# Optimization experiments

Hardware: AMD Instinct MI355X
Metric: run time of the kernel (lower is better)

The kernel has to match this reference:

```python
import jax, jax.numpy as jnp
import numpy as np


def _run_stacked_lstm(x, init_hc, params):
    """x: [B,T,E]; init_hc: tuple of (h,c) per layer; params: tuple of (W,U,b) per layer.
    Keras LSTMCell gate order: i, f, g(candidate), o; sigmoid recurrent act, tanh act."""
    def step(carry, xt):
        inp = xt
        new = []
        for (h, c), (W, U, b) in zip(carry, params):
            z = inp @ W + h @ U + b                      # [B, 4*units]
            i, f, g, o = jnp.split(z, 4, axis=-1)
            c2 = jax.nn.sigmoid(f) * c + jax.nn.sigmoid(i) * jnp.tanh(g)
            h2 = jax.nn.sigmoid(o) * jnp.tanh(c2)
            new.append((h2, c2))
            inp = h2                                     # feed to next layer
        return tuple(new), inp
    carry, ys = jax.lax.scan(step, init_hc, jnp.swapaxes(x, 0, 1))
    return jnp.swapaxes(ys, 0, 1), carry                 # [B,T,units], final states


def setup_inputs() -> dict:
    key = jax.random.key(0)
    ks = jax.random.split(key, 20)
    B, T, V, E, H, L = 16, 64, 32000, 512, 512, 2
    s = 0.02
    inp = {
        'ids_1': jax.random.randint(ks[0], (B, T), 0, V),
        'ids_2': jax.random.randint(ks[1], (B, T), 0, V),
        'init_state': jax.random.normal(ks[2], (L, B, H), jnp.float32),
        'emb': jax.random.normal(ks[3], (V, E), jnp.float32) * s,
        'W1_0': jax.random.normal(ks[4], (E, 4 * H), jnp.float32) * s,
        'U1_0': jax.random.normal(ks[5], (H, 4 * H), jnp.float32) * s,
        'b1_0': jnp.zeros((4 * H,), jnp.float32),
        'W1_1': jax.random.normal(ks[6], (H, 4 * H), jnp.float32) * s,
        'U1_1': jax.random.normal(ks[7], (H, 4 * H), jnp.float32) * s,
        'b1_1': jnp.zeros((4 * H,), jnp.float32),
        'W2_0': jax.random.normal(ks[8], (E, 8 * H), jnp.float32) * s,
        'U2_0': jax.random.normal(ks[9], (2 * H, 8 * H), jnp.float32) * s,
        'b2_0': jnp.zeros((8 * H,), jnp.float32),
        'W2_1': jax.random.normal(ks[10], (2 * H, 8 * H), jnp.float32) * s,
        'U2_1': jax.random.normal(ks[11], (2 * H, 8 * H), jnp.float32) * s,
        'b2_1': jnp.zeros((8 * H,), jnp.float32),
        'Wp1': jax.random.normal(ks[12], (H, V), jnp.float32) * s,
        'bp1': jnp.zeros((V,), jnp.float32),
        'Wp2': jax.random.normal(ks[13], (2 * H, V), jnp.float32) * s,
        'bp2': jnp.zeros((V,), jnp.float32),
    }
    return inp


def reference(ids_1, ids_2, init_state, emb,
              W1_0, U1_0, b1_0, W1_1, U1_1, b1_1,
              W2_0, U2_0, b2_0, W2_1, U2_1, b2_1,
              Wp1, bp1, Wp2, bp2):
    L = init_state.shape[0]
    e1 = emb[ids_1]                                       # [B,T,E]
    e2 = emb[ids_2]
    # RNN1: initial (h,c) both set to init_state per layer
    init1 = tuple((init_state[l], init_state[l]) for l in range(L))
    p1 = ((W1_0, U1_0, b1_0), (W1_1, U1_1, b1_1))
    out1, st1 = _run_stacked_lstm(e1, init1, p1)
    logits1 = out1 @ Wp1 + bp1                            # [B,T,V]
    # RNN2: initial h = concat(init, h1_final), c = concat(init, c1_final)
    init2 = tuple((jnp.concatenate([init_state[l], st1[l][0]], axis=1),
                   jnp.concatenate([init_state[l], st1[l][1]], axis=1))
                  for l in range(L))
    p2 = ((W2_0, U2_0, b2_0), (W2_1, U2_1, b2_1))
    out2, _ = _run_stacked_lstm(e2, init2, p2)
    logits2 = out2 @ Wp2 + bp2                            # [B,T,V]
    return (logits1, logits2)
```

## Files before the change

### kernel.cpp

```cpp
#include <hip/hip_runtime.h>
#include <hip/hip_bf16.h>

#define B_ 16
#define T_ 64
#define E_ 512
#define H_ 512
#define V_ 32000

typedef __attribute__((ext_vector_type(4))) float f32x4;
typedef __attribute__((ext_vector_type(8))) short s16x8;

__device__ __forceinline__ float sigm(float x){ return 1.0f/(1.0f + __expf(-x)); }

__device__ __forceinline__ unsigned short f2bf(float x){
  unsigned int u = __float_as_uint(x);
  return (unsigned short)((u + 0x7FFFu + ((u>>16)&1u)) >> 16);
}

__device__ __forceinline__ unsigned load_coh(const unsigned* p){
  unsigned v;
  asm volatile("global_load_dword %0, %1, off sc0 sc1\n\ts_waitcnt vmcnt(0)"
               : "=v"(v) : "v"(p) : "memory");
  return v;
}
__device__ __forceinline__ void store_coh16(unsigned short* p, unsigned v){
  asm volatile("global_store_short %0, %1, off sc0 sc1" :: "v"(p), "v"(v) : "memory");
}
__device__ __forceinline__ void store_cohf(float* p, float v){
  asm volatile("global_store_dword %0, %1, off sc0 sc1" :: "v"(p), "v"(v) : "memory");
}

__device__ __forceinline__ void gbar2(unsigned* barb, unsigned bi1,
                                      unsigned grp, unsigned grpcnt){
  asm volatile("s_waitcnt vmcnt(0)" ::: "memory");
  __syncthreads();
  if(threadIdx.x == 0){
    unsigned* ctr = barb + (size_t)grp*64;
    unsigned* mst = barb + (size_t)8*64;
    unsigned* gen = barb + (size_t)9*64;
    unsigned a = __hip_atomic_fetch_add(ctr, 1u, __ATOMIC_RELAXED, __HIP_MEMORY_SCOPE_AGENT);
    if(a == bi1*grpcnt - 1u){
      unsigned m = __hip_atomic_fetch_add(mst, 1u, __ATOMIC_RELAXED, __HIP_MEMORY_SCOPE_AGENT);
      if(m == bi1*8u - 1u){
        asm volatile("global_store_dword %0, %1, off sc0 sc1\n\ts_waitcnt vmcnt(0)"
                     :: "v"(gen), "v"(bi1) : "memory");
      }
    }
    while(load_coh(gen) < bi1) __builtin_amdgcn_s_sleep(1);
  }
  __syncthreads();
}

__global__ void k_barinit(unsigned* bar){
  int i = blockIdx.x*256 + threadIdx.x;
  if(i < 2048) bar[i] = 0u;
}

__global__ void k_gather(const int* __restrict__ ids, const float* __restrict__ emb,
                         unsigned short* __restrict__ out){
  const int row = blockIdx.x;
  const int id  = ids[row];
  float4 v = *(const float4*)(emb + (size_t)id*E_ + threadIdx.x*4);
  ushort4 o;
  o.x = f2bf(v.x); o.y = f2bf(v.y); o.z = f2bf(v.z); o.w = f2bf(v.w);
  *(ushort4*)(out + (size_t)row*E_ + threadIdx.x*4) = o;
}

__global__ __launch_bounds__(256)
void k_tcvt(const float* __restrict__ in, unsigned short* __restrict__ out,
            int N, int Hp, int Kfull, int koff, int swz){
  __shared__ float tile[32][33];
  const int n0 = blockIdx.x*32, k0 = blockIdx.y*32;
  const int x = threadIdx.x & 31, y = threadIdx.x >> 5;
  #pragma unroll
  for(int i=0;i<4;i++){
    int k = y + i*8;
    tile[k][x] = in[(size_t)(k0+k)*N + n0 + x];
  }
  __syncthreads();
  #pragma unroll
  for(int i=0;i<4;i++){
    int nl = y + i*8;
    int n  = n0 + nl;
    int p  = Hp ? ((n % Hp)*4 + n / Hp) : n;
    int kk = koff + k0 + x;
    size_t idx;
    if(swz){
      int k2 = kk*2;
      int slot = ((k2>>4)&7) ^ (p&7);
      idx = (size_t)p*Kfull + (((k2 & ~127) | (slot<<4) | (k2 & 15)) >> 1);
    } else {
      idx = (size_t)p*Kfull + kk;
    }
    out[idx] = f2bf(tile[x][nl]);
  }
}

__global__ void k_bpack(const float* __restrict__ b, float* __restrict__ out, int H, int N){
  int p = blockIdx.x*256 + threadIdx.x;
  if(p < N) out[p] = b[(p&3)*H + (p>>2)];
}

__global__ void k_init1(const float* __restrict__ init_state,
                        unsigned short* h0i, float* c0i, unsigned short* h1i, float* c1i){
  int i = blockIdx.x*256 + threadIdx.x;
  if(i >= B_*H_) return;
  float v0 = init_state[i];
  float v1 = init_state[B_*H_ + i];
  h0i[i] = f2bf(v0); c0i[i] = v0;
  h1i[i] = f2bf(v1); c1i[i] = v1;
}

__global__ void k_init2(const float* __restrict__ init_state,
                        const unsigned short* __restrict__ h0seq1,
                        const unsigned short* __restrict__ h1seq1,
                        const float* __restrict__ c0f1, const float* __restrict__ c1f1,
                        unsigned short* h20i, unsigned short* h21i,
                        float* c20i, float* c21i){
  const int l = blockIdx.y;
  int i = blockIdx.x*256 + threadIdx.x;
  if(i >= B_*2*H_) return;
  const int r = i >> 10, j = i & 1023;
  unsigned short* ho = l ? h21i : h20i;
  float* co = l ? c21i : c20i;
  if(j < H_){
    float v = init_state[(size_t)l*B_*H_ + r*H_ + j];
    ho[i] = f2bf(v); co[i] = v;
  } else {
    const unsigned short* hs = l ? h1seq1 : h0seq1;
    const float* cf = l ? c1f1 : c0f1;
    ho[i] = hs[(size_t)(r*T_ + (T_-1))*H_ + (j - H_)];
    co[i] = cf[r*H_ + (j - H_)];
  }
}

template<int BF32>
__global__ __launch_bounds__(256)
void k_mm(const unsigned short* __restrict__ A, const void* __restrict__ Bsrc,
          const float* __restrict__ bias, float* __restrict__ C,
          int M, int N, int K){
  __shared__ __align__(16) unsigned short As[128*64];
  __shared__ __align__(16) unsigned short Bs[128*64];
  const int tid = threadIdx.x;
  const int lane = tid & 63, w = tid >> 6;
  const int wm = (w>>1)*64, wn = (w&1)*64;
  const int bm = blockIdx.y*128, bn = blockIdx.x*128;
  const int l15 = lane & 15, kg = lane >> 4;
  f32x4 acc[4][4] = {};

  for(int k0=0; k0<K; k0+=64){
    __syncthreads();
    #pragma unroll
    for(int ch=0; ch<4; ch++){
      int off = ch*4096 + tid*16;
      int row = off >> 7;
      int s   = ((off >> 4) & 7) ^ (row & 7);
      __builtin_amdgcn_global_load_lds(
        (const __attribute__((address_space(1))) unsigned int*)(A + (size_t)(bm+row)*K + k0 + s*8),
        (__attribute__((address_space(3))) unsigned int*)((char*)As + off), 16, 0, 0);
    }
    if(BF32){
      const float* Bf = (const float*)Bsrc;
      #pragma unroll
      for(int i=0;i<8;i++){
        int kl = (tid>>5) + i*8;
        int nl = (tid&31)*4;
        float4 v = *(const float4*)(Bf + (size_t)(k0+kl)*N + bn + nl);
        int slot = kl >> 3, kb = kl & 7;
        float vv[4] = {v.x, v.y, v.z, v.w};
        #pragma unroll
        for(int jj=0;jj<4;jj++){
          int n = nl + jj;
          Bs[n*64 + ((slot ^ (n&7))*8) + kb] = f2bf(vv[jj]);
        }
      }
    } else {
      const unsigned short* Bt = (const unsigned short*)Bsrc;
      #pragma unroll
      for(int ch=0; ch<4; ch++){
        int off = ch*4096 + tid*16;
        int row = off >> 7;
        int s   = ((off >> 4) & 7) ^ (row & 7);
        __builtin_amdgcn_global_load_lds(
          (const __attribute__((address_space(1))) unsigned int*)(Bt + (size_t)(bn+row)*K + k0 + s*8),
          (__attribute__((address_space(3))) unsigned int*)((char*)Bs + off), 16, 0, 0);
      }
    }
    __syncthreads();

    #pragma unroll
    for(int q=0;q<2;q++){
      s16x8 af[4], bf[4];
      #pragma unroll
      for(int mt=0;mt<4;mt++){
        int row = wm + mt*16 + l15;
        int s = (q*4 + kg) ^ (row & 7);
        af[mt] = *(const s16x8*)(As + row*64 + s*8);
      }
      #pragma unroll
      for(int nt=0;nt<4;nt++){
        int row = wn + nt*16 + l15;
        int s = (q*4 + kg) ^ (row & 7);
        bf[nt] = *(const s16x8*)(Bs + row*64 + s*8);
      }
      #pragma unroll
      for(int mt=0;mt<4;mt++)
        #pragma unroll
        for(int nt=0;nt<4;nt++)
          acc[mt][nt] = __builtin_amdgcn_mfma_f32_16x16x32_bf16(af[mt], bf[nt], acc[mt][nt], 0, 0, 0);
    }
  }
  #pragma unroll
  for(int mt=0;mt<4;mt++){
    #pragma unroll
    for(int nt=0;nt<4;nt++){
      int col = bn + wn + nt*16 + l15;
      float bv = bias ? bias[col] : 0.f;
      #pragma unroll
      for(int e=0;e<4;e++){
        int row = bm + wm + mt*16 + kg*4 + e;
        C[(size_t)row*N + col] = acc[mt][nt][e] + bv;
      }
    }
  }
}

template<int C, int K, int LAYER, int HU>
__device__ __forceinline__ void rnn_body(
    unsigned short* __restrict__ Uld, float* __restrict__ zp,
    const unsigned short* __restrict__ Uslice,
    const float* __restrict__ xw0, const float* __restrict__ bpk,
    const unsigned short* __restrict__ h0init, const unsigned short* __restrict__ h1init,
    const float* __restrict__ cinit,
    unsigned short* __restrict__ h0seq, unsigned short* __restrict__ h1seq,
    float* __restrict__ cfin, unsigned* bar, int cb,
    unsigned grp, unsigned grpcnt)
{
  constexpr int KW = K/4, KS = KW/32, FR = C/16, UB = C/4;
  constexpr int K2 = K*2;
  constexpr int ITEMS = 16*UB;
  const int tid = threadIdx.x;
  const int lane = tid & 63, w = tid >> 6;
  const int l15 = lane & 15, kg = lane >> 4;

  constexpr int CP = (C*K2)/4096;
  #pragma unroll
  for(int i=0;i<CP;i++){
    __builtin_amdgcn_global_load_lds(
      (const __attribute__((address_space(1))) unsigned int*)((const char*)Uslice + i*4096 + tid*16),
      (__attribute__((address_space(3))) unsigned int*)((char*)Uld + i*4096 + tid*16), 16, 0, 0);
  }
  const int base_p = cb*C;
  const int base_u = cb*UB;
  float4 bvr = make_float4(0.f,0.f,0.f,0.f);
  int er = 0, eu = 0;
  if(tid < ITEMS){ er = tid / UB; eu = tid - er*UB; bvr = *(const float4*)(bpk + base_p + eu*4); }
  float creg = 0.f;
  unsigned short* hseqW = LAYER ? h1seq : h0seq;

  int cbyte[FR], cx[FR];
  #pragma unroll
  for(int f=0;f<FR;f++){ int c = f*16 + l15; cbyte[f] = c*K2; cx[f] = (c&7)<<4; }

  __syncthreads();

  for(int it = 0; it <= T_; ++it){
    const bool active = LAYER ? (it >= 1) : (it < T_);
    const int t = LAYER ? it-1 : it;
    if(active){
      const unsigned short* asrc;
      if constexpr(LAYER == 0){
        asrc = (t == 0) ? (h0init + l15*HU)
                        : (h0seq + ((size_t)(l15*T_ + (t-1)))*HU);
      } else {
        if(w < 2){
          asrc = h0seq + ((size_t)(l15*T_ + t))*HU;
        } else {
          asrc = ((t == 0) ? (h1init + l15*HU)
                           : (h1seq + ((size_t)(l15*T_ + (t-1)))*HU)) - HU;
        }
      }
      f32x4 acc[FR];
      #pragma unroll
      for(int f=0;f<FR;f++) acc[f] = (f32x4){0.f,0.f,0.f,0.f};
      #pragma unroll
      for(int s=0;s<KS;s++){
        const int kel = w*KW + s*32 + kg*8;
        s16x8 a = *(const s16x8*)(asrc + kel);
        const int kb  = kel*2;
        const int kch = kb & ~127;
        const int ksl = (kb >> 4) & 7;
        #pragma unroll
        for(int f=0;f<FR;f++){
          const int ad = cbyte[f] + kch + ((ksl<<4) ^ cx[f]);
          s16x8 b = *(const s16x8*)((const char*)Uld + ad);
          acc[f] = __builtin_amdgcn_mfma_f32_16x16x32_bf16(a, b, acc[f], 0, 0, 0);
        }
      }
      #pragma unroll
      for(int f=0;f<FR;f++)
        #pragma unroll
        for(int e=0;e<4;e++)
          zp[(w*16 + kg*4 + e)*68 + f*16 + l15] = acc[f][e];
    }
    __syncthreads();
    if(active && tid < ITEMS){
      float4 z0 = *(const float4*)(zp + (     er)*68 + eu*4);
      float4 z1 = *(const float4*)(zp + (16 + er)*68 + eu*4);
      float4 z2 = *(const float4*)(zp + (32 + er)*68 + eu*4);
      float4 z3 = *(const float4*)(zp + (48 + er)*68 + eu*4);
      float si = z0.x+z1.x+z2.x+z3.x + bvr.x;
      float sf = z0.y+z1.y+z2.y+z3.y + bvr.y;
      float sg = z0.z+z1.z+z2.z+z3.z + bvr.z;
      float so = z0.w+z1.w+z2.w+z3.w + bvr.w;
      if constexpr(LAYER == 0){
        float4 xv = *(const float4*)(xw0 + ((size_t)(er*T_ + t))*(4*HU) + base_p + eu*4);
        si += xv.x; sf += xv.y; sg += xv.z; so += xv.w;
      }
      float cin = (t == 0) ? cinit[er*HU + base_u + eu] : creg;
      float c2 = sigm(sf)*cin + sigm(si)*tanhf(sg);
      float h2 = sigm(so)*tanhf(c2);
      creg = c2;
      store_coh16(&hseqW[((size_t)(er*T_ + t))*HU + base_u + eu], (unsigned)f2bf(h2));
      if(t == T_-1) store_cohf(&cfin[er*HU + base_u + eu], c2);
    }
    if(it < T_) gbar2(bar, (unsigned)(it+1), grp, grpcnt);
  }
}

template<int HU, int C0, int C1>
__global__ __launch_bounds__(256, 1)
void k_rnn(const unsigned short* __restrict__ Ut0, const unsigned short* __restrict__ WU1,
           const float* __restrict__ xw0, const float* __restrict__ bpk0, const float* __restrict__ bpk1,
           const unsigned short* __restrict__ h0init, const unsigned short* __restrict__ h1init,
           const float* __restrict__ c0init, const float* __restrict__ c1init,
           unsigned short* __restrict__ h0seq, unsigned short* __restrict__ h1seq,
           float* __restrict__ c0fin, float* __restrict__ c1fin, unsigned* bar)
{
  constexpr int NB0 = 4*HU/C0;
  constexpr int UMAXE = (C0*HU > C1*2*HU) ? C0*HU : C1*2*HU;
  __shared__ __align__(16) unsigned short Uld[UMAXE];
  __shared__ __align__(16) float zred[64*68];
  const unsigned grp = blockIdx.x & 7u;
  const unsigned grpcnt = gridDim.x >> 3;
  const int blk = blockIdx.x;
  if(blk < NB0)
    rnn_body<C0, HU, 0, HU>(Uld, zred, Ut0 + (size_t)blk*C0*HU, xw0, bpk0,
                            h0init, h1init, c0init, h0seq, h1seq, c0fin, bar, blk, grp, grpcnt);
  else
    rnn_body<C1, 2*HU, 1, HU>(Uld, zred, WU1 + (size_t)(blk-NB0)*C1*2*HU, nullptr, bpk1,
                            h0init, h1init, c1init, h0seq, h1seq, c1fin, bar, blk-NB0, grp, grpcnt);
}

extern "C" void kernel_launch(void* const* d_in, const int* in_sizes, int n_in,
                              void* d_out, int out_size, void* d_ws, size_t ws_size,
                              hipStream_t stream){
  const int*   ids1 = (const int*)d_in[0];
  const int*   ids2 = (const int*)d_in[1];
  const float* init = (const float*)d_in[2];
  const float* emb  = (const float*)d_in[3];
  const float* W1_0 = (const float*)d_in[4];
  const float* U1_0 = (const float*)d_in[5];
  const float* b1_0 = (const float*)d_in[6];
  const float* W1_1 = (const float*)d_in[7];
  const float* U1_1 = (const float*)d_in[8];
  const float* b1_1 = (const float*)d_in[9];
  const float* W2_0 = (const float*)d_in[10];
  const float* U2_0 = (const float*)d_in[11];
  const float* b2_0 = (const float*)d_in[12];
  const float* W2_1 = (const float*)d_in[13];
  const float* U2_1 = (const float*)d_in[14];
  const float* b2_1 = (const float*)d_in[15];
  const float* Wp1  = (const float*)d_in[16];
  const float* bp1  = (const float*)d_in[17];
  const float* Wp2  = (const float*)d_in[18];
  const float* bp2  = (const float*)d_in[19];
  float* out1 = (float*)d_out;
  float* out2 = out1 + (size_t)B_*T_*V_;

  char* base = (char*)d_ws;
  float*          xw    = (float*)(base);
  unsigned short* ut0_1 = (unsigned short*)(base + (16u<<20));
  unsigned short* wu1_1 = (unsigned short*)(base + (18u<<20));
  unsigned short* ut0_2 = (unsigned short*)(base + (22u<<20));
  unsigned short* wu1_2 = (unsigned short*)(base + (30u<<20));
  unsigned short* wtmp  = (unsigned short*)(base + (46u<<20));
  unsigned short* ebuf  = (unsigned short*)(base + (50u<<20));
  unsigned short* h0s1  = (unsigned short*)(base + (51u<<20));
  unsigned short* h1s1  = (unsigned short*)(base + (52u<<20));
  unsigned short* h0s2  = (unsigned short*)(base + (53u<<20));
  unsigned short* h1s2  = (unsigned short*)(base + (55u<<20));
  char* M = base + (57u<<20);
  unsigned short* h0i1 = (unsigned short*)(M);
  unsigned short* h1i1 = (unsigned short*)(M + 16384);
  float* c0i1 = (float*)(M + 32768);
  float* c1i1 = (float*)(M + 65536);
  unsigned short* h2i0 = (unsigned short*)(M + 98304);
  unsigned short* h2i1 = (unsigned short*)(M + 131072);
  float* c2i0 = (float*)(M + 163840);
  float* c2i1 = (float*)(M + 229376);
  float* c0f1 = (float*)(M + 294912);
  float* c1f1 = (float*)(M + 327680);
  float* c0f2 = (float*)(M + 360448);
  float* c1f2 = (float*)(M + 425984);
  float* bpk10 = (float*)(M + 491520);
  float* bpk11 = (float*)(M + 499712);
  float* bpk20 = (float*)(M + 507904);
  float* bpk21 = (float*)(M + 524288);
  unsigned* bar1 = (unsigned*)(M + 540672);
  unsigned* bar2 = (unsigned*)(M + 544768);
  unsigned short* wpT = (unsigned short*)(base + (58u<<20));
  const size_t NEED_ALL = ((size_t)58u<<20) + (size_t)V_*1024*2;
  const bool wide = ws_size >= NEED_ALL;

  k_barinit<<<dim3(8), dim3(256), 0, stream>>>(bar1);

  k_init1<<<dim3(32), dim3(256), 0, stream>>>(init, h0i1, c0i1, h1i1, c1i1);
  k_gather<<<dim3(B_*T_), dim3(128), 0, stream>>>(ids1, emb, ebuf);
  k_tcvt<<<dim3(64, 16), dim3(256), 0, stream>>>(U1_0, ut0_1, 2048, 512, 512, 0, 1);
  k_tcvt<<<dim3(64, 16), dim3(256), 0, stream>>>(W1_0, wtmp,  2048, 512, 512, 0, 0);
  k_tcvt<<<dim3(64, 16), dim3(256), 0, stream>>>(W1_1, wu1_1, 2048, 512, 1024, 0, 1);
  k_tcvt<<<dim3(64, 16), dim3(256), 0, stream>>>(U1_1, wu1_1, 2048, 512, 1024, 512, 1);
  k_bpack<<<dim3(8),  dim3(256), 0, stream>>>(b1_0, bpk10, 512, 2048);
  k_bpack<<<dim3(8),  dim3(256), 0, stream>>>(b1_1, bpk11, 512, 2048);
  k_mm<0><<<dim3(16, 8), dim3(256), 0, stream>>>(ebuf, wtmp, nullptr, xw, 1024, 2048, 512);
  k_rnn<512, 64, 64><<<dim3(64), dim3(256), 0, stream>>>(ut0_1, wu1_1, xw, bpk10, bpk11,
      h0i1, h1i1, c0i1, c1i1, h0s1, h1s1, c0f1, c1f1, bar1);
  if(wide){
    k_tcvt<<<dim3(1000, 16), dim3(256), 0, stream>>>(Wp1, wpT, V_, 0, 512, 0, 0);
    k_mm<0><<<dim3(250, 8), dim3(256), 0, stream>>>(h1s1, wpT, bp1, out1, 1024, V_, 512);
  } else {
    k_mm<1><<<dim3(250, 8), dim3(256), 0, stream>>>(h1s1, Wp1, bp1, out1, 1024, V_, 512);
  }

  k_init2<<<dim3(64, 2), dim3(256), 0, stream>>>(init, h0s1, h1s1, c0f1, c1f1,
                                                 h2i0, h2i1, c2i0, c2i1);
  k_gather<<<dim3(B_*T_), dim3(128), 0, stream>>>(ids2, emb, ebuf);
  k_tcvt<<<dim3(128, 32), dim3(256), 0, stream>>>(U2_0, ut0_2, 4096, 1024, 1024, 0, 1);
  k_tcvt<<<dim3(128, 16), dim3(256), 0, stream>>>(W2_0, wtmp,  4096, 1024, 512, 0, 0);
  k_tcvt<<<dim3(128, 32), dim3(256), 0, stream>>>(W2_1, wu1_2, 4096, 1024, 2048, 0, 1);
  k_tcvt<<<dim3(128, 32), dim3(256), 0, stream>>>(U2_1, wu1_2, 4096, 1024, 2048, 1024, 1);
  k_bpack<<<dim3(16), dim3(256), 0, stream>>>(b2_0, bpk20, 1024, 4096);
  k_bpack<<<dim3(16), dim3(256), 0, stream>>>(b2_1, bpk21, 1024, 4096);
  k_mm<0><<<dim3(32, 8), dim3(256), 0, stream>>>(ebuf, wtmp, nullptr, xw, 1024, 4096, 512);
  k_rnn<1024, 64, 32><<<dim3(192), dim3(256), 0, stream>>>(ut0_2, wu1_2, xw, bpk20, bpk21,
      h2i0, h2i1, c2i0, c2i1, h0s2, h1s2, c0f2, c1f2, bar2);
  if(wide){
    k_tcvt<<<dim3(1000, 32), dim3(256), 0, stream>>>(Wp2, wpT, V_, 0, 1024, 0, 0);
    k_mm<0><<<dim3(250, 8), dim3(256), 0, stream>>>(h1s2, wpT, bp2, out2, 1024, V_, 1024);
  } else {
    k_mm<1><<<dim3(250, 8), dim3(256), 0, stream>>>(h1s2, Wp2, bp2, out2, 1024, V_, 1024);
  }
}
```

Measured before the change: 934.3 us.

## Replace grid-wide barrier with per-block progress flags and column-split recurrent GEMV

The global two-level atomic barrier between timesteps is replaced by per-block monotonic progress flags that consumers poll for just the producers they depend on. Layer 0 and layer 1 now advance as a dataflow pipeline instead of lockstep, with layer 1 waiting on layer 0's flag for the same step. Layer 0 and the small RNN's layer 1 also switch to a column-split scheme where each wave owns whole columns and gates are combined with lane shuffles, which removes the LDS split-K reduction and one __syncthreads per step. In exchange, every wave polls many flags with coherent loads, adding memory traffic and added complexity around ordering.

```diff
diff --git a/kernel.cpp b/kernel.cpp
--- a/kernel.cpp
+++ b/kernel.cpp
@@ -29,26 +29,22 @@
 __device__ __forceinline__ void store_cohf(float* p, float v){
   asm volatile("global_store_dword %0, %1, off sc0 sc1" :: "v"(p), "v"(v) : "memory");
 }
-
-__device__ __forceinline__ void gbar2(unsigned* barb, unsigned bi1,
-                                      unsigned grp, unsigned grpcnt){
-  asm volatile("s_waitcnt vmcnt(0)" ::: "memory");
-  __syncthreads();
-  if(threadIdx.x == 0){
-    unsigned* ctr = barb + (size_t)grp*64;
-    unsigned* mst = barb + (size_t)8*64;
-    unsigned* gen = barb + (size_t)9*64;
-    unsigned a = __hip_atomic_fetch_add(ctr, 1u, __ATOMIC_RELAXED, __HIP_MEMORY_SCOPE_AGENT);
-    if(a == bi1*grpcnt - 1u){
-      unsigned m = __hip_atomic_fetch_add(mst, 1u, __ATOMIC_RELAXED, __HIP_MEMORY_SCOPE_AGENT);
-      if(m == bi1*8u - 1u){
-        asm volatile("global_store_dword %0, %1, off sc0 sc1\n\ts_waitcnt vmcnt(0)"
-                     :: "v"(gen), "v"(bi1) : "memory");
-      }
-    }
-    while(load_coh(gen) < bi1) __builtin_amdgcn_s_sleep(1);
-  }
-  __syncthreads();
+__device__ __forceinline__ void store_cohu(unsigned* p, unsigned v){
+  asm volatile("global_store_dword %0, %1, off sc0 sc1" :: "v"(p), "v"(v) : "memory");
+}
+
+template<int NF>
+__device__ __forceinline__ void pollge(const unsigned* flags, unsigned target){
+  const int lane = threadIdx.x & 63;
+  if constexpr(NF <= 64){
+    const unsigned* p = flags + (lane % NF);
+    while(load_coh(p) < target) __builtin_amdgcn_s_sleep(1);
+  } else {
+    const unsigned* p0 = flags + lane;
+    const unsigned* p1 = flags + 64 + lane;
+    while(load_coh(p0) < target) __builtin_amdgcn_s_sleep(1);
+    while(load_coh(p1) < target) __builtin_amdgcn_s_sleep(1);
+  }
 }
 
 __global__ void k_barinit(unsigned* bar){
@@ -225,16 +221,110 @@
   }
 }
 
-template<int C, int K, int LAYER, int HU>
-__device__ __forceinline__ void rnn_body(
-    unsigned short* __restrict__ Uld, float* __restrict__ zp,
+template<int K, int LAYER, int HU, int NF0, int NF1>
+__device__ __forceinline__ void rnn_colsplit(
+    unsigned short* __restrict__ Uld,
     const unsigned short* __restrict__ Uslice,
     const float* __restrict__ xw0, const float* __restrict__ bpk,
     const unsigned short* __restrict__ h0init, const unsigned short* __restrict__ h1init,
     const float* __restrict__ cinit,
     unsigned short* __restrict__ h0seq, unsigned short* __restrict__ h1seq,
-    float* __restrict__ cfin, unsigned* bar, int cb,
-    unsigned grp, unsigned grpcnt)
+    float* __restrict__ cfin, unsigned* flag0, unsigned* flag1, int cb)
+{
+  constexpr int K2 = K*2;
+  constexpr int KS = K/32;
+  const int tid = threadIdx.x;
+  const int lane = tid & 63, w = tid >> 6;
+  const int l15 = lane & 15, kg = lane >> 4;
+
+  constexpr int CP = (64*K2)/4096;
+  #pragma unroll
+  for(int i=0;i<CP;i++){
+    __builtin_amdgcn_global_load_lds(
+      (const __attribute__((address_space(1))) unsigned int*)((const char*)Uslice + i*4096 + tid*16),
+      (__attribute__((address_space(3))) unsigned int*)((char*)Uld + i*4096 + tid*16), 16, 0, 0);
+  }
+  const int lc = w*16 + l15;
+  const int cbyte = lc*K2;
+  const int cx = (lc&7)<<4;
+  const bool act = ((l15 & 3) == 0);
+  const int gu = cb*16 + w*4 + (l15>>2);
+  const int p0 = gu*4;
+  unsigned short* hseqW = LAYER ? h1seq : h0seq;
+  unsigned* myflag = (LAYER ? flag1 : flag0) + cb;
+  float4 bv = act ? *(const float4*)(bpk + p0) : make_float4(0.f,0.f,0.f,0.f);
+  f32x4 creg = {};
+
+  __syncthreads();
+
+  for(int t = 0; t < T_; ++t){
+    float4 xv[4];
+    if(LAYER==0 && act){
+      #pragma unroll
+      for(int e=0;e<4;e++)
+        xv[e] = *(const float4*)(xw0 + ((size_t)((kg*4+e)*T_ + t))*(4*HU) + p0);
+    }
+    if(LAYER==0){ if(t>0) pollge<NF0>(flag0, (unsigned)t); }
+    else { pollge<NF0>(flag0, (unsigned)(t+1)); if(t>0) pollge<NF1>(flag1, (unsigned)t); }
+    const unsigned short* aA;
+    const unsigned short* aB = nullptr;
+    if constexpr(LAYER==0){
+      aA = (t==0) ? (h0init + l15*HU) : (h0seq + ((size_t)(l15*T_ + (t-1)))*HU);
+    } else {
+      aA = h0seq + ((size_t)(l15*T_ + t))*HU;
+      aB = (t==0) ? (h1init + l15*HU) : (h1seq + ((size_t)(l15*T_ + (t-1)))*HU);
+    }
+    f32x4 acc = {};
+    #pragma unroll
+    for(int s=0;s<KS;s++){
+      const int kel = s*32 + kg*8;
+      s16x8 a;
+      if constexpr(LAYER==0) a = *(const s16x8*)(aA + kel);
+      else a = (kel < HU) ? *(const s16x8*)(aA + kel) : *(const s16x8*)(aB + (kel - HU));
+      const int kb = kel*2;
+      const int ad = cbyte + (kb & ~127) + ((((kb>>4)&7)<<4) ^ cx);
+      s16x8 b = *(const s16x8*)((const char*)Uld + ad);
+      acc = __builtin_amdgcn_mfma_f32_16x16x32_bf16(a, b, acc, 0, 0, 0);
+    }
+    f32x4 zF_, zG_, zO_;
+    #pragma unroll
+    for(int e=0;e<4;e++){
+      zF_[e] = __shfl_xor(acc[e], 1, 64);
+      zG_[e] = __shfl_xor(acc[e], 2, 64);
+      zO_[e] = __shfl_xor(acc[e], 3, 64);
+    }
+    if(act){
+      #pragma unroll
+      for(int e=0;e<4;e++){
+        const int r = kg*4 + e;
+        float si = acc[e] + bv.x;
+        float sf = zF_[e] + bv.y;
+        float sg = zG_[e] + bv.z;
+        float so = zO_[e] + bv.w;
+        if constexpr(LAYER==0){ si += xv[e].x; sf += xv[e].y; sg += xv[e].z; so += xv[e].w; }
+        float cin = (t==0) ? cinit[r*HU + gu] : creg[e];
+        float c2 = sigm(sf)*cin + sigm(si)*tanhf(sg);
+        float h2 = sigm(so)*tanhf(c2);
+        creg[e] = c2;
+        store_coh16(&hseqW[((size_t)(r*T_ + t))*HU + gu], (unsigned)f2bf(h2));
+        if(t == T_-1) store_cohf(&cfin[r*HU + gu], c2);
+      }
+    }
+    asm volatile("s_waitcnt vmcnt(0)" ::: "memory");
+    __syncthreads();
+    if(tid == 0) store_cohu(myflag, (unsigned)(t+1));
+  }
+}
+
+template<int C, int K, int HU, int NF0, int NF1>
+__device__ __forceinline__ void rnn_splitk1(
+    unsigned short* __restrict__ Uld, float* __restrict__ zp,
+    const unsigned short* __restrict__ Uslice,
+    const float* __restrict__ bpk,
+    const unsigned short* __restrict__ h1init,
+    const float* __restrict__ cinit,
+    unsigned short* __restrict__ h0seq, unsigned short* __restrict__ h1seq,
+    float* __restrict__ cfin, unsigned* flag0, unsigned* flag1, int cb)
 {
   constexpr int KW = K/4, KS = KW/32, FR = C/16, UB = C/4;
   constexpr int K2 = K*2;
@@ -256,7 +346,6 @@
   int er = 0, eu = 0;
   if(tid < ITEMS){ er = tid / UB; eu = tid - er*UB; bvr = *(const float4*)(bpk + base_p + eu*4); }
   float creg = 0.f;
-  unsigned short* hseqW = LAYER ? h1seq : h0seq;
 
   int cbyte[FR], cx[FR];
   #pragma unroll
@@ -264,47 +353,37 @@
 
   __syncthreads();
 
-  for(int it = 0; it <= T_; ++it){
-    const bool active = LAYER ? (it >= 1) : (it < T_);
-    const int t = LAYER ? it-1 : it;
-    if(active){
-      const unsigned short* asrc;
-      if constexpr(LAYER == 0){
-        asrc = (t == 0) ? (h0init + l15*HU)
-                        : (h0seq + ((size_t)(l15*T_ + (t-1)))*HU);
-      } else {
-        if(w < 2){
-          asrc = h0seq + ((size_t)(l15*T_ + t))*HU;
-        } else {
-          asrc = ((t == 0) ? (h1init + l15*HU)
-                           : (h1seq + ((size_t)(l15*T_ + (t-1)))*HU)) - HU;
-        }
-      }
-      f32x4 acc[FR];
-      #pragma unroll
-      for(int f=0;f<FR;f++) acc[f] = (f32x4){0.f,0.f,0.f,0.f};
-      #pragma unroll
-      for(int s=0;s<KS;s++){
-        const int kel = w*KW + s*32 + kg*8;
-        s16x8 a = *(const s16x8*)(asrc + kel);
-        const int kb  = kel*2;
-        const int kch = kb & ~127;
-        const int ksl = (kb >> 4) & 7;
-        #pragma unroll
-        for(int f=0;f<FR;f++){
-          const int ad = cbyte[f] + kch + ((ksl<<4) ^ cx[f]);
-          s16x8 b = *(const s16x8*)((const char*)Uld + ad);
-          acc[f] = __builtin_amdgcn_mfma_f32_16x16x32_bf16(a, b, acc[f], 0, 0, 0);
-        }
-      }
-      #pragma unroll
-      for(int f=0;f<FR;f++)
-        #pragma unroll
-        for(int e=0;e<4;e++)
-          zp[(w*16 + kg*4 + e)*68 + f*16 + l15] = acc[f][e];
-    }
+  for(int t = 0; t < T_; ++t){
+    if(w < 2) pollge<NF0>(flag0, (unsigned)(t+1));
+    else if(t > 0) pollge<NF1>(flag1, (unsigned)t);
+    const unsigned short* asrc;
+    if(w < 2) asrc = h0seq + ((size_t)(l15*T_ + t))*HU;
+    else asrc = ((t==0) ? (h1init + l15*HU)
+                        : (h1seq + ((size_t)(l15*T_ + (t-1)))*HU)) - HU;
+    f32x4 acc[FR];
+    #pragma unroll
+    for(int f=0;f<FR;f++) acc[f] = (f32x4){0.f,0.f,0.f,0.f};
+    #pragma unroll
+    for(int s=0;s<KS;s++){
+      const int kel = w*KW + s*32 + kg*8;
+      s16x8 a = *(const s16x8*)(asrc + kel);
+      const int kb  = kel*2;
+      const int kch = kb & ~127;
+      const int ksl = (kb >> 4) & 7;
+      #pragma unroll
+      for(int f=0;f<FR;f++){
+        const int ad = cbyte[f] + kch + ((ksl<<4) ^ cx[f]);
+        s16x8 b = *(const s16x8*)((const char*)Uld + ad);
+        acc[f] = __builtin_amdgcn_mfma_f32_16x16x32_bf16(a, b, acc[f], 0, 0, 0);
+      }
+    }
+    #pragma unroll
+    for(int f=0;f<FR;f++)
+      #pragma unroll
+      for(int e=0;e<4;e++)
+        zp[(w*16 + kg*4 + e)*68 + f*16 + l15] = acc[f][e];
     __syncthreads();
-    if(active && tid < ITEMS){
+    if(tid < ITEMS){
       float4 z0 = *(const float4*)(zp + (     er)*68 + eu*4);
       float4 z1 = *(const float4*)(zp + (16 + er)*68 + eu*4);
       float4 z2 = *(const float4*)(zp + (32 + er)*68 + eu*4);
@@ -313,22 +392,20 @@
       float sf = z0.y+z1.y+z2.y+z3.y + bvr.y;
       float sg = z0.z+z1.z+z2.z+z3.z + bvr.z;
       float so = z0.w+z1.w+z2.w+z3.w + bvr.w;
-      if constexpr(LAYER == 0){
-        float4 xv = *(const float4*)(xw0 + ((size_t)(er*T_ + t))*(4*HU) + base_p + eu*4);
-        si += xv.x; sf += xv.y; sg += xv.z; so += xv.w;
-      }
-      float cin = (t == 0) ? cinit[er*HU + base_u + eu] : creg;
+      float cin = (t==0) ? cinit[er*HU + base_u + eu] : creg;
       float c2 = sigm(sf)*cin + sigm(si)*tanhf(sg);
       float h2 = sigm(so)*tanhf(c2);
       creg = c2;
-      store_coh16(&hseqW[((size_t)(er*T_ + t))*HU + base_u + eu], (unsigned)f2bf(h2));
+      store_coh16(&h1seq[((size_t)(er*T_ + t))*HU + base_u + eu], (unsigned)f2bf(h2));
       if(t == T_-1) store_cohf(&cfin[er*HU + base_u + eu], c2);
     }
-    if(it < T_) gbar2(bar, (unsigned)(it+1), grp, grpcnt);
-  }
-}
-
-template<int HU, int C0, int C1>
+    asm volatile("s_waitcnt vmcnt(0)" ::: "memory");
+    __syncthreads();
+    if(tid == 0) store_cohu(flag1 + cb, (unsigned)(t+1));
+  }
+}
+
+template<int HU, int C1>
 __global__ __launch_bounds__(256, 1)
 void k_rnn(const unsigned short* __restrict__ Ut0, const unsigned short* __restrict__ WU1,
            const float* __restrict__ xw0, const float* __restrict__ bpk0, const float* __restrict__ bpk1,
@@ -337,19 +414,24 @@
            unsigned short* __restrict__ h0seq, unsigned short* __restrict__ h1seq,
            float* __restrict__ c0fin, float* __restrict__ c1fin, unsigned* bar)
 {
-  constexpr int NB0 = 4*HU/C0;
-  constexpr int UMAXE = (C0*HU > C1*2*HU) ? C0*HU : C1*2*HU;
+  constexpr int NB0 = 4*HU/64;
+  constexpr int NB1 = 4*HU/C1;
+  constexpr int UMAXE = (64*HU > C1*2*HU) ? 64*HU : C1*2*HU;
   __shared__ __align__(16) unsigned short Uld[UMAXE];
   __shared__ __align__(16) float zred[64*68];
-  const unsigned grp = blockIdx.x & 7u;
-  const unsigned grpcnt = gridDim.x >> 3;
+  unsigned* flag0 = bar;
+  unsigned* flag1 = bar + 128;
   const int blk = blockIdx.x;
-  if(blk < NB0)
-    rnn_body<C0, HU, 0, HU>(Uld, zred, Ut0 + (size_t)blk*C0*HU, xw0, bpk0,
-                            h0init, h1init, c0init, h0seq, h1seq, c0fin, bar, blk, grp, grpcnt);
-  else
-    rnn_body<C1, 2*HU, 1, HU>(Uld, zred, WU1 + (size_t)(blk-NB0)*C1*2*HU, nullptr, bpk1,
-                            h0init, h1init, c1init, h0seq, h1seq, c1fin, bar, blk-NB0, grp, grpcnt);
+  if(blk < NB0){
+    rnn_colsplit<HU, 0, HU, NB0, NB1>(Uld, Ut0 + (size_t)blk*64*HU, xw0, bpk0,
+        h0init, h1init, c0init, h0seq, h1seq, c0fin, flag0, flag1, blk);
+  } else if constexpr(C1 == 64){
+    rnn_colsplit<2*HU, 1, HU, NB0, NB1>(Uld, WU1 + (size_t)(blk-NB0)*64*2*HU, nullptr, bpk1,
+        h0init, h1init, c1init, h0seq, h1seq, c1fin, flag0, flag1, blk-NB0);
+  } else {
+    rnn_splitk1<C1, 2*HU, HU, NB0, NB1>(Uld, zred, WU1 + (size_t)(blk-NB0)*C1*2*HU, bpk1,
+        h1init, c1init, h0seq, h1seq, c1fin, flag0, flag1, blk-NB0);
+  }
 }
 
 extern "C" void kernel_launch(void* const* d_in, const int* in_sizes, int n_in,
@@ -424,7 +506,7 @@
   k_bpack<<<dim3(8),  dim3(256), 0, stream>>>(b1_0, bpk10, 512, 2048);
   k_bpack<<<dim3(8),  dim3(256), 0, stream>>>(b1_1, bpk11, 512, 2048);
   k_mm<0><<<dim3(16, 8), dim3(256), 0, stream>>>(ebuf, wtmp, nullptr, xw, 1024, 2048, 512);
-  k_rnn<512, 64, 64><<<dim3(64), dim3(256), 0, stream>>>(ut0_1, wu1_1, xw, bpk10, bpk11,
+  k_rnn<512, 64><<<dim3(64), dim3(256), 0, stream>>>(ut0_1, wu1_1, xw, bpk10, bpk11,
       h0i1, h1i1, c0i1, c1i1, h0s1, h1s1, c0f1, c1f1, bar1);
   if(wide){
     k_tcvt<<<dim3(1000, 16), dim3(256), 0, stream>>>(Wp1, wpT, V_, 0, 512, 0, 0);
@@ -443,7 +525,7 @@
   k_bpack<<<dim3(16), dim3(256), 0, stream>>>(b2_0, bpk20, 1024, 4096);
   k_bpack<<<dim3(16), dim3(256), 0, stream>>>(b2_1, bpk21, 1024, 4096);
   k_mm<0><<<dim3(32, 8), dim3(256), 0, stream>>>(ebuf, wtmp, nullptr, xw, 1024, 4096, 512);
-  k_rnn<1024, 64, 32><<<dim3(192), dim3(256), 0, stream>>>(ut0_2, wu1_2, xw, bpk20, bpk21,
+  k_rnn<1024, 32><<<dim3(192), dim3(256), 0, stream>>>(ut0_2, wu1_2, xw, bpk20, bpk21,
       h2i0, h2i1, c2i0, c2i1, h0s2, h1s2, c0f2, c1f2, bar2);
   if(wide){
     k_tcvt<<<dim3(1000, 32), dim3(256), 0, stream>>>(Wp2, wpT, V_, 0, 1024, 0, 0);
```

Result: slower. 1.384 ms (+48.2%).
